# Kernel optimization log

Hardware: AMD Instinct MI355X
Metric: run time of the kernel (lower is better)

The kernel has to match this reference:

```python
import jax, jax.numpy as jnp
import numpy as np

N_NODES = 100000


def gcn_conv(x, src, dst, W, b):
    """PyG GCNConv: add self-loops, symmetric D^-1/2 (A+I) D^-1/2 normalization.
    x: [N, Fin]; src/dst: [E'] (self-loops already appended); W: [Fin, Fout]; b: [Fout].
    """
    xw = x @ W  # [N, Fout]
    ones = jnp.ones(dst.shape[0], dtype=x.dtype)
    deg = jax.ops.segment_sum(ones, dst, num_segments=N_NODES)  # in-degree incl. self-loop
    dinv = jnp.where(deg > 0, jax.lax.rsqrt(deg), 0.0)
    norm = dinv[src] * dinv[dst]  # [E']
    msg = xw[src] * norm[:, None]  # gather + scale
    out = jax.ops.segment_sum(msg, dst, num_segments=N_NODES)  # scatter-add
    return out + b


def setup_inputs() -> dict:
    key = jax.random.key(0)
    ks = jax.random.split(key, 12)
    hidden = 64
    E = 1600000
    x_node = jax.random.normal(ks[0], (N_NODES, 1), dtype=jnp.float32)
    edge_index = jax.random.randint(ks[1], (2, E), 0, N_NODES, dtype=jnp.int64)

    def glorot(k, fan_in, fan_out):
        lim = float(np.sqrt(6.0 / (fan_in + fan_out)))
        return jax.random.uniform(k, (fan_in, fan_out), jnp.float32, -lim, lim)

    W1 = glorot(ks[2], 1, hidden)
    b1 = jnp.zeros((hidden,), jnp.float32)
    W2 = glorot(ks[3], hidden, hidden)
    b2 = jnp.zeros((hidden,), jnp.float32)
    W3 = glorot(ks[4], hidden, hidden)
    b3 = jnp.zeros((hidden,), jnp.float32)
    W4 = glorot(ks[5], hidden, 1)
    b4 = jnp.zeros((1,), jnp.float32)
    return {"x_node": x_node, "edge_index": edge_index,
            "W1": W1, "b1": b1, "W2": W2, "b2": b2,
            "W3": W3, "b3": b3, "W4": W4, "b4": b4}


def reference(x_node, edge_index, W1, b1, W2, b2, W3, b3, W4, b4):
    # Append self-loops once (shared by both GCN layers, as PyG does per-layer with identical result)
    loops = jnp.arange(N_NODES, dtype=edge_index.dtype)
    src = jnp.concatenate([edge_index[0], loops])
    dst = jnp.concatenate([edge_index[1], loops])

    h = jax.nn.silu(gcn_conv(x_node, src, dst, W1, b1))
    h = jax.nn.silu(gcn_conv(h, src, dst, W2, b2))
    h = jax.nn.silu(h @ W3 + b3)
    return h @ W4 + b4  # [N, 1]
```

## Files before the change

### kernel.cpp

```cpp
#include <hip/hip_runtime.h>
#include <math.h>

#define N_NODES 100000
#define NPB    196
#define NBUCK  511
#define CAP    3584
#define CHUNKA 2048

#define NCHEB  12
#define SMAX   6.0f

__device__ __forceinline__ float silu_f(float x) {
    return x * __builtin_amdgcn_rcpf(1.0f + __builtin_amdgcn_exp2f(-1.442695041f * x));
}

__device__ __forceinline__ float bcast_f(float v, int lane) {
    return __int_as_float(__builtin_amdgcn_readlane(__float_as_int(v), lane));
}

__global__ __launch_bounds__(512) void k_bucket(const int* __restrict__ src,
                                                const int* __restrict__ dst,
                                                int* __restrict__ gcur,
                                                unsigned int* __restrict__ buf,
                                                const float* __restrict__ W1,
                                                const float* __restrict__ b1,
                                                float* __restrict__ cheb, int E) {
    __shared__ unsigned hist[512];
    __shared__ unsigned lbase[512];
    __shared__ unsigned gbase[512];
    __shared__ unsigned lcur[512];
    __shared__ unsigned wtot[8];
    __shared__ unsigned pay[CHUNKA];
    __shared__ unsigned short bkt[CHUNKA];
    int t = threadIdx.x;
    int lane = t & 63, wid = t >> 6;
    hist[t] = 0;
    __syncthreads();
    int e0 = blockIdx.x * CHUNKA;
    int e1 = min(e0 + CHUNKA, E);
    for (int e = e0 + t; e < e1; e += 512)
        atomicAdd(&hist[dst[e] / NPB], 1u);
    __syncthreads();
    unsigned v = hist[t], sc = v;
#pragma unroll
    for (int off = 1; off < 64; off <<= 1) {
        unsigned y = __shfl_up(sc, off, 64);
        if (lane >= off) sc += y;
    }
    if (lane == 63) wtot[wid] = sc;
    __syncthreads();
    unsigned add = 0;
    for (int w = 0; w < wid; ++w) add += wtot[w];
    unsigned ex = sc - v + add;
    lbase[t] = ex;
    gbase[t] = v ? (unsigned)atomicAdd(&gcur[t], (int)v) : 0u;
    lcur[t] = 0;
    __syncthreads();
    for (int e = e0 + t; e < e1; e += 512) {
        int d = dst[e];
        int s = src[e];
        int b = d / NPB;
        unsigned pos = lbase[b] + atomicAdd(&lcur[b], 1u);
        pay[pos] = ((unsigned)s << 8) | (unsigned)(d - b * NPB);
        bkt[pos] = (unsigned short)b;
    }
    __syncthreads();
    int cb = e1 - e0;
    for (int i = t; i < cb; i += 512) {
        int b = bkt[i];
        unsigned gp = gbase[b] + ((unsigned)i - lbase[b]);
        if (gp < CAP)
            buf[(size_t)b * CAP + gp] = pay[i];
    }

    if (blockIdx.x == 0 && t < 64) {
        int f = t;
        float w = W1[f], b = b1[f];
        float g[NCHEB], th[NCHEB];
        const float pi = 3.14159265358979f;
#pragma unroll
        for (int j = 0; j < NCHEB; ++j) {
            th[j] = (j + 0.5f) * (pi / NCHEB);
            float S = SMAX * __cosf(th[j]);
            float y = fmaf(w, S, b);
            g[j] = y / (1.0f + expf(-y));
        }
#pragma unroll
        for (int k = 0; k < NCHEB; ++k) {
            float s = 0.f;
#pragma unroll
            for (int j = 0; j < NCHEB; ++j)
                s += g[j] * __cosf((float)k * th[j]);
            cheb[k * 64 + f] = s * ((k == 0) ? (1.0f / NCHEB) : (2.0f / NCHEB));
        }
    }
}

__global__ __launch_bounds__(512) void k_build(const int* __restrict__ gcur,
                                               unsigned int* __restrict__ buf,
                                               const float* __restrict__ x,
                                               int* __restrict__ rowptr,
                                               int* __restrict__ cnt,
                                               float* __restrict__ dinv,
                                               float* __restrict__ xs, int N) {
    __shared__ unsigned hist[256];
    __shared__ unsigned cur[256];
    __shared__ unsigned wtot[4];
    __shared__ unsigned lsrc[CAP];
    int b = blockIdx.x;
    int t = threadIdx.x;
    int lane = t & 63, wid = t >> 6;
    int cb = min(gcur[b], CAP);
    int n0 = b * NPB;
    int np = min(N - n0, NPB);
    unsigned int* bb = buf + (size_t)b * CAP;

    if (t < 256) hist[t] = 0;
    __syncthreads();
    for (int i = t; i < cb; i += 512) atomicAdd(&hist[bb[i] & 255u], 1u);
    __syncthreads();
    unsigned v = (t < 256) ? hist[t] : 0u, sc = v;
#pragma unroll
    for (int off = 1; off < 64; off <<= 1) {
        unsigned y = __shfl_up(sc, off, 64);
        if (lane >= off) sc += y;
    }
    if (lane == 63 && t < 256) wtot[wid] = sc;
    __syncthreads();
    unsigned add = 0;
    for (int w = 0; w < wid && w < 4; ++w) add += wtot[w];
    unsigned ex = sc - v + add;
    if (t < 256) cur[t] = ex;
    if (t < np) {
        int node = n0 + t;
        int deg = (int)v;
        cnt[node] = deg;
        rowptr[node] = b * CAP + (int)ex;
        float dv = rsqrtf((float)(deg + 1));
        dinv[node] = dv;
        xs[node] = x[node] * dv;
    }
    __syncthreads();
    for (int i = t; i < cb; i += 512) {
        unsigned p = bb[i];
        unsigned pos = atomicAdd(&cur[p & 255u], 1u);
        lsrc[pos] = p >> 8;
    }
    __syncthreads();
    for (int i = t; i < cb; i += 512) bb[i] = lsrc[i];
}

__global__ __launch_bounds__(256) void k_sd(const int* __restrict__ rowptr,
                                            const int* __restrict__ cnt,
                                            const int* __restrict__ csr,
                                            const float* __restrict__ xs,
                                            const float* __restrict__ dinv,
                                            float2* __restrict__ sd, int N) {
    int t = blockIdx.x * 256 + threadIdx.x;
    int i = t >> 3, sub = t & 7;
    if (i >= N) return;
    int start = rowptr[i], deg = cnt[i];
    float sum = 0.f;
    int ia = (sub < deg) ? csr[start + sub] : -1;
    int ib = (sub + 8 < deg) ? csr[start + sub + 8] : -1;
    if (ia >= 0) sum += xs[ia];
    if (ib >= 0) sum += xs[ib];
    for (int j = sub + 16; j < deg; j += 8) sum += xs[csr[start + j]];
    sum += __shfl_xor(sum, 1, 64);
    sum += __shfl_xor(sum, 2, 64);
    sum += __shfl_xor(sum, 4, 64);
    if (sub == 0) {
        float d = dinv[i];
        sd[i] = make_float2((sum + xs[i]) * d, d);
    }
}

__global__ __launch_bounds__(256, 8) void k_final(
    const int* __restrict__ rowptr, const int* __restrict__ cnt,
    const int* __restrict__ csr, const float2* __restrict__ sd,
    const float* __restrict__ cheb,
    const float* __restrict__ W2, const float* __restrict__ b2,
    const float* __restrict__ W3, const float* __restrict__ b3,
    const float* __restrict__ W4, const float* __restrict__ b4,
    float* __restrict__ out, int N)
{
    __shared__ float sA[64 * 65];
    __shared__ float sP[4 * 64];

    const int lane = threadIdx.x & 63;
    const int wid  = __builtin_amdgcn_readfirstlane(threadIdx.x >> 6);
    const int tile0 = blockIdx.x * 64;
    const int nbase = tile0 + wid * 16;
    const int row0  = wid * 16;

    const int nloc = lane >> 2, sub = lane & 3;
    const int i = nbase + nloc;
    const bool valid = (i < N);
    int start = 0, deg = 0;
    float2 self = make_float2(0.f, 0.f);
    if (valid) {
        start = rowptr[i];
        deg   = cnt[i];
        self  = sd[i];
    }

    float m[NCHEB];
    {
        float d = (sub == 0) ? self.y : 0.f;
        float t = fminf(fmaxf(self.x * (1.0f / SMAX), -1.f), 1.f);
        float t2 = t + t, Tm = 1.f, Tc = t;
        m[0] = d;
        m[1] = d * t;
#pragma unroll
        for (int k = 2; k < NCHEB; ++k) {
            float Tn = fmaf(t2, Tc, -Tm);
            m[k] = d * Tn;
            Tm = Tc; Tc = Tn;
        }
    }

    int uu[8];
    float2 sv[8];
#pragma unroll
    for (int q = 0; q < 8; ++q) {
        int j = sub + 4 * q;
        uu[q] = (j < deg) ? csr[start + j] : -1;
    }
#pragma unroll
    for (int q = 0; q < 8; ++q) {
        sv[q] = (uu[q] >= 0) ? sd[uu[q]] : make_float2(0.f, 0.f);
    }
#pragma unroll
    for (int q = 0; q < 8; ++q) {
        if (uu[q] >= 0) {
            float d = sv[q].y;
            float t = fminf(fmaxf(sv[q].x * (1.0f / SMAX), -1.f), 1.f);
            float t2 = t + t, Tm = 1.f, Tc = t;
            m[0] += d;
            m[1] = fmaf(d, t, m[1]);
#pragma unroll
            for (int k = 2; k < NCHEB; ++k) {
                float Tn = fmaf(t2, Tc, -Tm);
                m[k] = fmaf(d, Tn, m[k]);
                Tm = Tc; Tc = Tn;
            }
        }
    }
    for (int j = sub + 32; j < deg; j += 4) {
        int u = csr[start + j];
        float2 su = sd[u];
        float d = su.y;
        float t = fminf(fmaxf(su.x * (1.0f / SMAX), -1.f), 1.f);
        float t2 = t + t, Tm = 1.f, Tc = t;
        m[0] += d;
        m[1] = fmaf(d, t, m[1]);
#pragma unroll
        for (int k = 2; k < NCHEB; ++k) {
            float Tn = fmaf(t2, Tc, -Tm);
            m[k] = fmaf(d, Tn, m[k]);
            Tm = Tc; Tc = Tn;
        }
    }
#pragma unroll
    for (int k = 0; k < NCHEB; ++k) {
        m[k] += __shfl_xor(m[k], 1, 64);
        m[k] += __shfl_xor(m[k], 2, 64);
    }

    float ck[NCHEB];
#pragma unroll
    for (int k = 0; k < NCHEB; ++k) ck[k] = cheb[k * 64 + lane];
#pragma unroll
    for (int nl = 0; nl < 16; ++nl) {
        float acc = 0.f;
#pragma unroll
        for (int k = 0; k < NCHEB; ++k)
            acc = fmaf(ck[k], bcast_f(m[k], 4 * nl), acc);
        float dv = bcast_f(self.y, 4 * nl);
        sA[(row0 + nl) * 65 + lane] = acc * dv;
    }
    __syncthreads();

    const int f0 = wid * 16;
    float acc2[16];
#pragma unroll
    for (int j = 0; j < 16; ++j) acc2[j] = b2[f0 + j];
    for (int k = 0; k < 64; ++k) {
        float av = sA[lane * 65 + k];
#pragma unroll
        for (int j = 0; j < 16; ++j)
            acc2[j] = fmaf(av, W2[k * 64 + f0 + j], acc2[j]);
    }
    __syncthreads();
#pragma unroll
    for (int j = 0; j < 16; ++j)
        sA[lane * 65 + f0 + j] = silu_f(acc2[j]);
    __syncthreads();

    float acc3[16];
#pragma unroll
    for (int j = 0; j < 16; ++j) acc3[j] = b3[f0 + j];
    for (int k = 0; k < 64; ++k) {
        float uv = sA[lane * 65 + k];
#pragma unroll
        for (int j = 0; j < 16; ++j)
            acc3[j] = fmaf(uv, W3[k * 64 + f0 + j], acc3[j]);
    }
    float part = 0.f;
#pragma unroll
    for (int j = 0; j < 16; ++j)
        part = fmaf(silu_f(acc3[j]), W4[f0 + j], part);
    sP[wid * 64 + lane] = part;
    __syncthreads();

    if (wid == 0) {
        int i2 = tile0 + lane;
        if (i2 < N)
            out[i2] = sP[lane] + sP[64 + lane] + sP[128 + lane] + sP[192 + lane] + b4[0];
    }
}

extern "C" void kernel_launch(void* const* d_in, const int* in_sizes, int n_in,
                              void* d_out, int out_size, void* d_ws, size_t ws_size,
                              hipStream_t stream) {
    const float* x  = (const float*)d_in[0];
    const int* edge = (const int*)d_in[1];
    const float* W1 = (const float*)d_in[2];
    const float* b1 = (const float*)d_in[3];
    const float* W2 = (const float*)d_in[4];
    const float* b2 = (const float*)d_in[5];
    const float* W3 = (const float*)d_in[6];
    const float* b3 = (const float*)d_in[7];
    const float* W4 = (const float*)d_in[8];
    const float* b4 = (const float*)d_in[9];
    float* out = (float*)d_out;

    const int N = N_NODES;
    const int E = in_sizes[1] / 2;
    const int* src = edge;
    const int* dst = edge + E;
    const int NCHUNK = (E + CHUNKA - 1) / CHUNKA;

    char* ws = (char*)d_ws;
    size_t off = 0;
    int*    gcur   = (int*)(ws + off);    off += 512 * 4;
    float2* sd     = (float2*)(ws + off); off += (size_t)N * 8;
    int*    rowptr = (int*)(ws + off);    off += (size_t)N * 4;
    int*    cnt    = (int*)(ws + off);    off += (size_t)N * 4;
    float*  dinv   = (float*)(ws + off);  off += (size_t)N * 4;
    float*  xs     = (float*)(ws + off);  off += (size_t)N * 4;
    float*  cheb   = (float*)(ws + off);  off += NCHEB * 64 * 4;
    unsigned int* buf = (unsigned int*)(ws + off); off += (size_t)NBUCK * CAP * 4;
    int* csr = (int*)buf;

    hipMemsetAsync(gcur, 0, 512 * 4, stream);

    k_bucket<<<NCHUNK, 512, 0, stream>>>(src, dst, gcur, buf, W1, b1, cheb, E);
    k_build <<<NBUCK, 512, 0, stream>>>(gcur, buf, x, rowptr, cnt, dinv, xs, N);
    k_sd    <<<(N * 8 + 255) / 256, 256, 0, stream>>>(rowptr, cnt, csr, xs, dinv, sd, N);
    k_final <<<(N + 63) / 64, 256, 0, stream>>>(rowptr, cnt, csr, sd, cheb,
                                                W2, b2, W3, b3, W4, b4, out, N);
}
```

Before: 160.3 us.

## Replace per-node CSR build with bucketed shared-memory atomic aggregation

```diff
diff --git a/kernel.cpp b/kernel.cpp
--- a/kernel.cpp
+++ b/kernel.cpp
@@ -2,20 +2,16 @@
 #include <math.h>
 
 #define N_NODES 100000
-#define NPB    196
-#define NBUCK  511
-#define CAP    3584
-#define CHUNKA 2048
+#define NPB    392
+#define NBUCK  256
+#define CAP    7168
+#define CHUNKA 4096
 
 #define NCHEB  12
 #define SMAX   6.0f
 
 __device__ __forceinline__ float silu_f(float x) {
     return x * __builtin_amdgcn_rcpf(1.0f + __builtin_amdgcn_exp2f(-1.442695041f * x));
-}
-
-__device__ __forceinline__ float bcast_f(float v, int lane) {
-    return __int_as_float(__builtin_amdgcn_readlane(__float_as_int(v), lane));
 }
 
 __global__ __launch_bounds__(512) void k_bucket(const int* __restrict__ src,
@@ -25,47 +21,60 @@
                                                 const float* __restrict__ W1,
                                                 const float* __restrict__ b1,
                                                 float* __restrict__ cheb, int E) {
-    __shared__ unsigned hist[512];
-    __shared__ unsigned lbase[512];
-    __shared__ unsigned gbase[512];
-    __shared__ unsigned lcur[512];
-    __shared__ unsigned wtot[8];
+    __shared__ unsigned hist[256];
+    __shared__ unsigned lbase[256];
+    __shared__ unsigned gbase[256];
+    __shared__ unsigned lcur[256];
+    __shared__ unsigned wtot[4];
     __shared__ unsigned pay[CHUNKA];
-    __shared__ unsigned short bkt[CHUNKA];
-    int t = threadIdx.x;
-    int lane = t & 63, wid = t >> 6;
-    hist[t] = 0;
-    __syncthreads();
-    int e0 = blockIdx.x * CHUNKA;
-    int e1 = min(e0 + CHUNKA, E);
-    for (int e = e0 + t; e < e1; e += 512)
-        atomicAdd(&hist[dst[e] / NPB], 1u);
-    __syncthreads();
-    unsigned v = hist[t], sc = v;
+    __shared__ unsigned char bkt[CHUNKA];
+    const int t = threadIdx.x;
+    const int lane = t & 63, wid = t >> 6;
+    if (t < 256) hist[t] = 0;
+    __syncthreads();
+    const int e0 = blockIdx.x * CHUNKA;
+    const int e1 = min(e0 + CHUNKA, E);
+
+    int sR[8], dR[8], bR[8];
+#pragma unroll
+    for (int q = 0; q < 8; ++q) {
+        int e = e0 + t + q * 512;
+        if (e < e1) {
+            dR[q] = dst[e];
+            sR[q] = src[e];
+            bR[q] = dR[q] / NPB;
+            atomicAdd(&hist[bR[q]], 1u);
+        } else bR[q] = -1;
+    }
+    __syncthreads();
+    unsigned v = (t < 256) ? hist[t] : 0u, sc = v;
 #pragma unroll
     for (int off = 1; off < 64; off <<= 1) {
         unsigned y = __shfl_up(sc, off, 64);
         if (lane >= off) sc += y;
     }
-    if (lane == 63) wtot[wid] = sc;
+    if (lane == 63 && t < 256) wtot[wid] = sc;
     __syncthreads();
     unsigned add = 0;
-    for (int w = 0; w < wid; ++w) add += wtot[w];
+    for (int w = 0; w < wid && w < 4; ++w) add += wtot[w];
     unsigned ex = sc - v + add;
-    lbase[t] = ex;
-    gbase[t] = v ? (unsigned)atomicAdd(&gcur[t], (int)v) : 0u;
-    lcur[t] = 0;
-    __syncthreads();
-    for (int e = e0 + t; e < e1; e += 512) {
-        int d = dst[e];
-        int s = src[e];
-        int b = d / NPB;
-        unsigned pos = lbase[b] + atomicAdd(&lcur[b], 1u);
-        pay[pos] = ((unsigned)s << 8) | (unsigned)(d - b * NPB);
-        bkt[pos] = (unsigned short)b;
-    }
-    __syncthreads();
-    int cb = e1 - e0;
+    if (t < 256) {
+        lbase[t] = ex;
+        gbase[t] = v ? (unsigned)atomicAdd(&gcur[t], (int)v) : 0u;
+        lcur[t] = 0;
+    }
+    __syncthreads();
+#pragma unroll
+    for (int q = 0; q < 8; ++q) {
+        if (bR[q] >= 0) {
+            int b = bR[q];
+            unsigned pos = lbase[b] + atomicAdd(&lcur[b], 1u);
+            pay[pos] = ((unsigned)sR[q] << 9) | (unsigned)(dR[q] - b * NPB);
+            bkt[pos] = (unsigned char)b;
+        }
+    }
+    __syncthreads();
+    const int cb = e1 - e0;
     for (int i = t; i < cb; i += 512) {
         int b = bkt[i];
         unsigned gp = gbase[b] + ((unsigned)i - lbase[b]);
@@ -96,88 +105,136 @@
     }
 }
 
-__global__ __launch_bounds__(512) void k_build(const int* __restrict__ gcur,
-                                               unsigned int* __restrict__ buf,
-                                               const float* __restrict__ x,
-                                               int* __restrict__ rowptr,
-                                               int* __restrict__ cnt,
-                                               float* __restrict__ dinv,
-                                               float* __restrict__ xs, int N) {
-    __shared__ unsigned hist[256];
-    __shared__ unsigned cur[256];
-    __shared__ unsigned wtot[4];
-    __shared__ unsigned lsrc[CAP];
-    int b = blockIdx.x;
-    int t = threadIdx.x;
-    int lane = t & 63, wid = t >> 6;
-    int cb = min(gcur[b], CAP);
-    int n0 = b * NPB;
-    int np = min(N - n0, NPB);
-    unsigned int* bb = buf + (size_t)b * CAP;
-
-    if (t < 256) hist[t] = 0;
-    __syncthreads();
-    for (int i = t; i < cb; i += 512) atomicAdd(&hist[bb[i] & 255u], 1u);
-    __syncthreads();
-    unsigned v = (t < 256) ? hist[t] : 0u, sc = v;
-#pragma unroll
-    for (int off = 1; off < 64; off <<= 1) {
-        unsigned y = __shfl_up(sc, off, 64);
-        if (lane >= off) sc += y;
-    }
-    if (lane == 63 && t < 256) wtot[wid] = sc;
-    __syncthreads();
-    unsigned add = 0;
-    for (int w = 0; w < wid && w < 4; ++w) add += wtot[w];
-    unsigned ex = sc - v + add;
-    if (t < 256) cur[t] = ex;
+__global__ __launch_bounds__(512) void k_deg(const int* __restrict__ gcur,
+                                             const unsigned int* __restrict__ buf,
+                                             const float* __restrict__ x,
+                                             float* __restrict__ dinv,
+                                             float* __restrict__ xs, int N) {
+    __shared__ unsigned hist[512];
+    const int b = blockIdx.x, t = threadIdx.x;
+    const int cb = min(gcur[b], CAP);
+    const unsigned int* bb = buf + (size_t)b * CAP;
+    hist[t] = 0;
+    __syncthreads();
+    for (int i = t; i < cb; i += 512) atomicAdd(&hist[bb[i] & 511u], 1u);
+    __syncthreads();
+    const int n0 = b * NPB;
+    const int np = min(N - n0, NPB);
     if (t < np) {
-        int node = n0 + t;
-        int deg = (int)v;
-        cnt[node] = deg;
-        rowptr[node] = b * CAP + (int)ex;
-        float dv = rsqrtf((float)(deg + 1));
-        dinv[node] = dv;
-        xs[node] = x[node] * dv;
-    }
-    __syncthreads();
-    for (int i = t; i < cb; i += 512) {
+        float dv = rsqrtf((float)(hist[t] + 1u));
+        dinv[n0 + t] = dv;
+        xs[n0 + t] = x[n0 + t] * dv;
+    }
+}
+
+__global__ __launch_bounds__(512) void k_agg(const int* __restrict__ gcur,
+                                             const unsigned int* __restrict__ buf,
+                                             const float* __restrict__ xs,
+                                             const float* __restrict__ dinv,
+                                             float2* __restrict__ sd, int N) {
+    __shared__ float ssum[512];
+    const int b = blockIdx.x, t = threadIdx.x;
+    const int cb = min(gcur[b], CAP);
+    const unsigned int* bb = buf + (size_t)b * CAP;
+    ssum[t] = 0.f;
+    __syncthreads();
+    int i = t;
+    for (; i + 1536 < cb; i += 2048) {
+        unsigned p0 = bb[i], p1 = bb[i + 512], p2 = bb[i + 1024], p3 = bb[i + 1536];
+        float v0 = xs[p0 >> 9], v1 = xs[p1 >> 9], v2 = xs[p2 >> 9], v3 = xs[p3 >> 9];
+        atomicAdd(&ssum[p0 & 511u], v0);
+        atomicAdd(&ssum[p1 & 511u], v1);
+        atomicAdd(&ssum[p2 & 511u], v2);
+        atomicAdd(&ssum[p3 & 511u], v3);
+    }
+    for (; i < cb; i += 512) {
         unsigned p = bb[i];
-        unsigned pos = atomicAdd(&cur[p & 255u], 1u);
-        lsrc[pos] = p >> 8;
-    }
-    __syncthreads();
-    for (int i = t; i < cb; i += 512) bb[i] = lsrc[i];
-}
-
-__global__ __launch_bounds__(256) void k_sd(const int* __restrict__ rowptr,
-                                            const int* __restrict__ cnt,
-                                            const int* __restrict__ csr,
-                                            const float* __restrict__ xs,
-                                            const float* __restrict__ dinv,
-                                            float2* __restrict__ sd, int N) {
-    int t = blockIdx.x * 256 + threadIdx.x;
-    int i = t >> 3, sub = t & 7;
-    if (i >= N) return;
-    int start = rowptr[i], deg = cnt[i];
-    float sum = 0.f;
-    int ia = (sub < deg) ? csr[start + sub] : -1;
-    int ib = (sub + 8 < deg) ? csr[start + sub + 8] : -1;
-    if (ia >= 0) sum += xs[ia];
-    if (ib >= 0) sum += xs[ib];
-    for (int j = sub + 16; j < deg; j += 8) sum += xs[csr[start + j]];
-    sum += __shfl_xor(sum, 1, 64);
-    sum += __shfl_xor(sum, 2, 64);
-    sum += __shfl_xor(sum, 4, 64);
-    if (sub == 0) {
-        float d = dinv[i];
-        sd[i] = make_float2((sum + xs[i]) * d, d);
+        atomicAdd(&ssum[p & 511u], xs[p >> 9]);
+    }
+    __syncthreads();
+    const int n0 = b * NPB;
+    const int np = min(N - n0, NPB);
+    if (t < np) {
+        float dv = dinv[n0 + t];
+        sd[n0 + t] = make_float2((ssum[t] + xs[n0 + t]) * dv, dv);
+    }
+}
+
+__global__ __launch_bounds__(512) void k_mom(const int* __restrict__ gcur,
+                                             const unsigned int* __restrict__ buf,
+                                             const float2* __restrict__ sd,
+                                             float* __restrict__ mom, int N) {
+    __shared__ float msum[NPB * NCHEB];
+    const int b = blockIdx.x, t = threadIdx.x;
+    const int cb = min(gcur[b], CAP);
+    const unsigned int* bb = buf + (size_t)b * CAP;
+    for (int j = t; j < NPB * NCHEB; j += 512) msum[j] = 0.f;
+    __syncthreads();
+
+    int i = t;
+    for (; i + 1536 < cb; i += 2048) {
+        unsigned p[4] = { bb[i], bb[i + 512], bb[i + 1024], bb[i + 1536] };
+        float2 sv[4];
+#pragma unroll
+        for (int q = 0; q < 4; ++q) sv[q] = sd[p[q] >> 9];
+#pragma unroll
+        for (int q = 0; q < 4; ++q) {
+            int dl = (int)(p[q] & 511u);
+            float d = sv[q].y;
+            float tt = fminf(fmaxf(sv[q].x * (1.0f / SMAX), -1.f), 1.f);
+            float t2 = tt + tt, Tm = 1.f, Tc = tt;
+            atomicAdd(&msum[dl * NCHEB + 0], d);
+            atomicAdd(&msum[dl * NCHEB + 1], d * tt);
+#pragma unroll
+            for (int k = 2; k < NCHEB; ++k) {
+                float Tn = fmaf(t2, Tc, -Tm);
+                atomicAdd(&msum[dl * NCHEB + k], d * Tn);
+                Tm = Tc; Tc = Tn;
+            }
+        }
+    }
+    for (; i < cb; i += 512) {
+        unsigned p = bb[i];
+        int dl = (int)(p & 511u);
+        float2 su = sd[p >> 9];
+        float d = su.y;
+        float tt = fminf(fmaxf(su.x * (1.0f / SMAX), -1.f), 1.f);
+        float t2 = tt + tt, Tm = 1.f, Tc = tt;
+        atomicAdd(&msum[dl * NCHEB + 0], d);
+        atomicAdd(&msum[dl * NCHEB + 1], d * tt);
+#pragma unroll
+        for (int k = 2; k < NCHEB; ++k) {
+            float Tn = fmaf(t2, Tc, -Tm);
+            atomicAdd(&msum[dl * NCHEB + k], d * Tn);
+            Tm = Tc; Tc = Tn;
+        }
+    }
+    __syncthreads();
+
+    const int n0 = b * NPB;
+    const int np = min(N - n0, NPB);
+    if (t < np) {
+        float2 si = sd[n0 + t];
+        float d = si.y;
+        float tt = fminf(fmaxf(si.x * (1.0f / SMAX), -1.f), 1.f);
+        float t2 = tt + tt, Tm = 1.f, Tc = tt;
+        float mloc[NCHEB];
+        mloc[0] = msum[t * NCHEB + 0] + d;
+        mloc[1] = msum[t * NCHEB + 1] + d * tt;
+#pragma unroll
+        for (int k = 2; k < NCHEB; ++k) {
+            float Tn = fmaf(t2, Tc, -Tm);
+            mloc[k] = msum[t * NCHEB + k] + d * Tn;
+            Tm = Tc; Tc = Tn;
+        }
+#pragma unroll
+        for (int k = 0; k < NCHEB; ++k)
+            mom[(size_t)k * N + n0 + t] = mloc[k];
     }
 }
 
 __global__ __launch_bounds__(256, 8) void k_final(
-    const int* __restrict__ rowptr, const int* __restrict__ cnt,
-    const int* __restrict__ csr, const float2* __restrict__ sd,
+    const float* __restrict__ dinv, const float* __restrict__ mom,
     const float* __restrict__ cheb,
     const float* __restrict__ W2, const float* __restrict__ b2,
     const float* __restrict__ W3, const float* __restrict__ b3,
@@ -186,98 +243,33 @@
 {
     __shared__ float sA[64 * 65];
     __shared__ float sP[4 * 64];
+    __shared__ float sM[64 * 13];
+    __shared__ float sD[64];
 
     const int lane = threadIdx.x & 63;
     const int wid  = __builtin_amdgcn_readfirstlane(threadIdx.x >> 6);
     const int tile0 = blockIdx.x * 64;
-    const int nbase = tile0 + wid * 16;
     const int row0  = wid * 16;
 
-    const int nloc = lane >> 2, sub = lane & 3;
-    const int i = nbase + nloc;
-    const bool valid = (i < N);
-    int start = 0, deg = 0;
-    float2 self = make_float2(0.f, 0.f);
-    if (valid) {
-        start = rowptr[i];
-        deg   = cnt[i];
-        self  = sd[i];
-    }
-
-    float m[NCHEB];
     {
-        float d = (sub == 0) ? self.y : 0.f;
-        float t = fminf(fmaxf(self.x * (1.0f / SMAX), -1.f), 1.f);
-        float t2 = t + t, Tm = 1.f, Tc = t;
-        m[0] = d;
-        m[1] = d * t;
-#pragma unroll
-        for (int k = 2; k < NCHEB; ++k) {
-            float Tn = fmaf(t2, Tc, -Tm);
-            m[k] = d * Tn;
-            Tm = Tc; Tc = Tn;
-        }
-    }
-
-    int uu[8];
-    float2 sv[8];
-#pragma unroll
-    for (int q = 0; q < 8; ++q) {
-        int j = sub + 4 * q;
-        uu[q] = (j < deg) ? csr[start + j] : -1;
-    }
-#pragma unroll
-    for (int q = 0; q < 8; ++q) {
-        sv[q] = (uu[q] >= 0) ? sd[uu[q]] : make_float2(0.f, 0.f);
-    }
-#pragma unroll
-    for (int q = 0; q < 8; ++q) {
-        if (uu[q] >= 0) {
-            float d = sv[q].y;
-            float t = fminf(fmaxf(sv[q].x * (1.0f / SMAX), -1.f), 1.f);
-            float t2 = t + t, Tm = 1.f, Tc = t;
-            m[0] += d;
-            m[1] = fmaf(d, t, m[1]);
-#pragma unroll
-            for (int k = 2; k < NCHEB; ++k) {
-                float Tn = fmaf(t2, Tc, -Tm);
-                m[k] = fmaf(d, Tn, m[k]);
-                Tm = Tc; Tc = Tn;
-            }
-        }
-    }
-    for (int j = sub + 32; j < deg; j += 4) {
-        int u = csr[start + j];
-        float2 su = sd[u];
-        float d = su.y;
-        float t = fminf(fmaxf(su.x * (1.0f / SMAX), -1.f), 1.f);
-        float t2 = t + t, Tm = 1.f, Tc = t;
-        m[0] += d;
-        m[1] = fmaf(d, t, m[1]);
-#pragma unroll
-        for (int k = 2; k < NCHEB; ++k) {
-            float Tn = fmaf(t2, Tc, -Tm);
-            m[k] = fmaf(d, Tn, m[k]);
-            Tm = Tc; Tc = Tn;
-        }
-    }
-#pragma unroll
-    for (int k = 0; k < NCHEB; ++k) {
-        m[k] += __shfl_xor(m[k], 1, 64);
-        m[k] += __shfl_xor(m[k], 2, 64);
-    }
-
+        int i = tile0 + lane;
+        for (int kk = wid; kk < NCHEB; kk += 4)
+            sM[lane * 13 + kk] = (i < N) ? mom[(size_t)kk * N + i] : 0.f;
+        if (wid == 0) sD[lane] = (i < N) ? dinv[i] : 0.f;
+    }
     float ck[NCHEB];
 #pragma unroll
     for (int k = 0; k < NCHEB; ++k) ck[k] = cheb[k * 64 + lane];
+    __syncthreads();
+
 #pragma unroll
     for (int nl = 0; nl < 16; ++nl) {
+        int row = row0 + nl;
         float acc = 0.f;
 #pragma unroll
         for (int k = 0; k < NCHEB; ++k)
-            acc = fmaf(ck[k], bcast_f(m[k], 4 * nl), acc);
-        float dv = bcast_f(self.y, 4 * nl);
-        sA[(row0 + nl) * 65 + lane] = acc * dv;
+            acc = fmaf(ck[k], sM[row * 13 + k], acc);
+        sA[row * 65 + lane] = acc * sD[row];
     }
     __syncthreads();
 
@@ -343,21 +335,20 @@
 
     char* ws = (char*)d_ws;
     size_t off = 0;
-    int*    gcur   = (int*)(ws + off);    off += 512 * 4;
-    float2* sd     = (float2*)(ws + off); off += (size_t)N * 8;
-    int*    rowptr = (int*)(ws + off);    off += (size_t)N * 4;
-    int*    cnt    = (int*)(ws + off);    off += (size_t)N * 4;
-    float*  dinv   = (float*)(ws + off);  off += (size_t)N * 4;
-    float*  xs     = (float*)(ws + off);  off += (size_t)N * 4;
-    float*  cheb   = (float*)(ws + off);  off += NCHEB * 64 * 4;
+    int*    gcur = (int*)(ws + off);    off += 256 * 4;
+    float*  dinv = (float*)(ws + off);  off += (size_t)N * 4;
+    float*  xs   = (float*)(ws + off);  off += (size_t)N * 4;
+    float2* sd   = (float2*)(ws + off); off += (size_t)N * 8;
+    float*  cheb = (float*)(ws + off);  off += NCHEB * 64 * 4;
+    float*  mom  = (float*)(ws + off);  off += (size_t)NCHEB * N * 4;
     unsigned int* buf = (unsigned int*)(ws + off); off += (size_t)NBUCK * CAP * 4;
-    int* csr = (int*)buf;
-
-    hipMemsetAsync(gcur, 0, 512 * 4, stream);
+
+    hipMemsetAsync(gcur, 0, 256 * 4, stream);
 
     k_bucket<<<NCHUNK, 512, 0, stream>>>(src, dst, gcur, buf, W1, b1, cheb, E);
-    k_build <<<NBUCK, 512, 0, stream>>>(gcur, buf, x, rowptr, cnt, dinv, xs, N);
-    k_sd    <<<(N * 8 + 255) / 256, 256, 0, stream>>>(rowptr, cnt, csr, xs, dinv, sd, N);
-    k_final <<<(N + 63) / 64, 256, 0, stream>>>(rowptr, cnt, csr, sd, cheb,
+    k_deg   <<<NBUCK, 512, 0, stream>>>(gcur, buf, x, dinv, xs, N);
+    k_agg   <<<NBUCK, 512, 0, stream>>>(gcur, buf, xs, dinv, sd, N);
+    k_mom   <<<NBUCK, 512, 0, stream>>>(gcur, buf, sd, mom, N);
+    k_final <<<(N + 63) / 64, 256, 0, stream>>>(dinv, mom, cheb,
                                                 W2, b2, W3, b3, W4, b4, out, N);
 }
```

After: 241.3 us. 1.51x slower.
